# Kernel optimization log

Measured on AMD Instinct MI355X. Metric: run time of the kernel, lower is better.

## Reference

```python
import jax, jax.numpy as jnp
import numpy as np

B, LQ, LP, H = 16, 2048, 2048, 1024

def setup_inputs() -> dict:
    key = jax.random.key(0)
    kq, kp, kw = jax.random.split(key, 3)
    q = jax.random.normal(kq, (B, LQ, H), dtype=jnp.float32)
    p = jax.random.normal(kp, (B, LP, H), dtype=jnp.float32)
    W = jax.random.normal(kw, (H, H), dtype=jnp.float32) * (1.0 / np.sqrt(H))
    b = jnp.zeros((H,), dtype=jnp.float32)
    return {"q": q, "p": p, "W": W, "b": b}

def reference(q, p, W, b):
    # shared linear + ReLU projections (torch Linear: x @ W.T + b)
    q_lin = jax.nn.relu(jnp.einsum('bqh,oh->bqo', q, W) + b)  # [B,LQ,H]
    p_lin = jax.nn.relu(jnp.einsum('bph,oh->bpo', p, W) + b)  # [B,LP,H]
    # unscaled cross-attention scores: p_lin @ q_lin^T -> [B,LP,LQ]
    scores = jnp.einsum('bpd,bqd->bpq', p_lin, q_lin)
    att = jax.nn.softmax(scores, axis=2)
    # context-aware query: att @ q_lin -> [B,LP,H]
    return jnp.einsum('bpq,bqd->bpd', att, q_lin)
```

## Files before the change

### kernel.cpp

```cpp
#include <hip/hip_runtime.h>


#define LQN 2048
#define LPN 2048
#define HD  1024
#define NBATCH 16

typedef _Float16 half8 __attribute__((ext_vector_type(8)));
typedef _Float16 half4_t __attribute__((ext_vector_type(4)));
typedef float f32x4 __attribute__((ext_vector_type(4)));

#define GLP(src, dst) __builtin_amdgcn_global_load_lds(                          \
    (const __attribute__((address_space(1))) void*)(src),                        \
    (__attribute__((address_space(3))) void*)(dst), 16, 0, 0)

__global__ __launch_bounds__(256) void cvt_f32_f16(const float* __restrict__ in,
                                                   _Float16* __restrict__ out,
                                                   long n4) {
  long i0 = (long)blockIdx.x * blockDim.x + threadIdx.x;
  long stride = (long)gridDim.x * blockDim.x;
  for (long i = i0; i < n4; i += stride) {
    float4 v = ((const float4*)in)[i];
    half4_t h = {(_Float16)v.x, (_Float16)v.y, (_Float16)v.z, (_Float16)v.w};
    ((half4_t*)out)[i] = h;
  }
}

__global__ __launch_bounds__(256) void transpose_k(const _Float16* __restrict__ in,
                                                   _Float16* __restrict__ out) {
  __shared__ _Float16 t[64][72];
  const int bz = blockIdx.z;
  const int q0 = blockIdx.x * 64;
  const int d0 = blockIdx.y * 64;
  const int tt = threadIdx.x;
  const int ql = tt & 63, dg = tt >> 6;
  const _Float16* src = in + ((size_t)bz * LQN + q0 + ql) * HD + d0 + dg * 16;
  half8 v0 = *(const half8*)(src);
  half8 v1 = *(const half8*)(src + 8);
  int g0 = (dg * 2) ^ (ql & 7);
  int g1 = (dg * 2 + 1) ^ (ql & 7);
  *(half8*)&t[ql][g0 * 8] = v0;
  *(half8*)&t[ql][g1 * 8] = v1;
  __syncthreads();
  const int dl = tt & 63, qg = tt >> 6;
  half8 o0, o1;
#pragma unroll
  for (int j = 0; j < 8; ++j) {
    int qq = qg * 16 + j;
    o0[j] = t[qq][(((dl >> 3) ^ (qq & 7)) << 3) + (dl & 7)];
  }
#pragma unroll
  for (int j = 0; j < 8; ++j) {
    int qq = qg * 16 + 8 + j;
    o1[j] = t[qq][(((dl >> 3) ^ (qq & 7)) << 3) + (dl & 7)];
  }
  _Float16* dst = out + ((size_t)bz * HD + d0 + dl) * LQN + q0 + qg * 16;
  *(half8*)dst = o0;
  *(half8*)(dst + 8) = o1;
}


#define SYNC_PRE                                        \
  __builtin_amdgcn_s_barrier();                         \
  __builtin_amdgcn_s_setprio(1);

#define SYNC_POST                                       \
  __builtin_amdgcn_s_setprio(0);                        \
  __builtin_amdgcn_s_barrier();                         \
  __builtin_amdgcn_sched_barrier(0);

#define SYNC_POST_VM                                    \
  __builtin_amdgcn_s_setprio(0);                        \
  asm volatile("s_waitcnt vmcnt(4)" ::: "memory");      \
  __builtin_amdgcn_s_barrier();                         \
  __builtin_amdgcn_sched_barrier(0);

#define LOADA_TO(dst, qm, buf)                                                    \
  _Pragma("unroll")                                                               \
  for (int mi = 0; mi < 4; ++mi) {                                                \
    dst[mi][0] = *(const half8*)(smA + (buf)*32768 + a0 + ((qm)*4+mi)*4096);      \
    dst[mi][1] = *(const half8*)(smA + (buf)*32768 + a1 + ((qm)*4+mi)*4096);      \
  }

#define LOADB_TO(dst, qn, buf)                                                    \
  _Pragma("unroll")                                                               \
  for (int ni = 0; ni < 2; ++ni) {                                                \
    dst[ni][0] = *(const half8*)(smB + (buf)*32768 + b0 + ((qn)*2+ni)*8192);      \
    dst[ni][1] = *(const half8*)(smB + (buf)*32768 + b1 + ((qn)*2+ni)*8192);      \
  }

#define STAGEA(t, h, buf) do {                                                    \
  GLP(gA + (size_t)((h)*128)*lda + (size_t)(t)*64,                                \
      smW + (buf)*32768 + (h)*16384 + wid*1024);                                  \
  GLP(gA + (size_t)((h)*128+64)*lda + (size_t)(t)*64,                             \
      smW + (buf)*32768 + (h)*16384 + 8192 + wid*1024);                           \
} while (0)

#define STAGEB(t, h, buf) do {                                                    \
  GLP(gB + (size_t)((h)*128)*ldb + (size_t)(t)*64,                                \
      smW + 65536 + (buf)*32768 + (h)*16384 + wid*1024);                          \
  GLP(gB + (size_t)((h)*128+64)*ldb + (size_t)(t)*64,                             \
      smW + 65536 + (buf)*32768 + (h)*16384 + 8192 + wid*1024);                   \
} while (0)

#define DO_MFMA2(aset, bset, qm, qn)                                              \
  _Pragma("unroll")                                                               \
  for (int mi = 0; mi < 4; ++mi) {                                                \
    _Pragma("unroll")                                                             \
    for (int ni = 0; ni < 2; ++ni) {                                              \
      acc[(qm)*4+mi][(qn)*2+ni] = __builtin_amdgcn_mfma_f32_16x16x32_f16(         \
          aset[mi][0], bset[ni][0], acc[(qm)*4+mi][(qn)*2+ni], 0, 0, 0);          \
      acc[(qm)*4+mi][(qn)*2+ni] = __builtin_amdgcn_mfma_f32_16x16x32_f16(         \
          aset[mi][1], bset[ni][1], acc[(qm)*4+mi][(qn)*2+ni], 0, 0, 0);          \
    }                                                                             \
  }

template <int EPI>
__global__ __launch_bounds__(512, 2) void gemm8p(
    const _Float16* __restrict__ A, const _Float16* __restrict__ B,
    const float* __restrict__ bias, void* __restrict__ Cv,
    float2* __restrict__ side, int K, int lda, int ldb, int ldc,
    long sAz, long sBz, long sCz) {
  extern __shared__ __align__(16) char smem[];
  const char* smA = smem;
  const char* smB = smem + 65536;
  char* smW = smem;

  const int tid = threadIdx.x;
  const int lane = tid & 63, wid = tid >> 6;
  const int l16 = lane & 15, lhi = lane >> 4;
  const int wr = wid >> 2, wcn = wid & 3;

  const int nx = gridDim.x;
  const int d = blockIdx.y * nx + blockIdx.x;
  const int cpx = (nx * gridDim.y) >> 3;
  const int t_ = (d & 7) * cpx + (d >> 3);
  const int xsh = 31 - __builtin_clz(nx);
  const int bn0 = (t_ & (nx - 1)) << 8;
  const int bm0 = (t_ >> xsh) << 8;

  const int mask = (l16 & 7) << 4;
  const int a0 = (wr * 2048 + l16 * 128 + lhi * 16) ^ mask;
  const int a1 = a0 ^ 64;
  const int b0 = (wcn * 2048 + l16 * 128 + lhi * 16) ^ mask;
  const int b1 = b0 ^ 64;

  const int srow = tid >> 3;
  const int scol = (((tid & 7) ^ ((tid >> 3) & 7)) << 3);

  const _Float16* gA = A + (size_t)blockIdx.z * sAz + (size_t)(bm0 + srow) * lda + scol;
  const _Float16* gB = B + (size_t)blockIdx.z * sBz + (size_t)(bn0 + srow) * ldb + scol;

  const int NT = K >> 6, NI = K >> 7;

  f32x4 acc[8][4] = {};
  half8 aA[4][2], bs0[2][2], bs1[2][2];

  STAGEA(0, 0, 0); STAGEA(0, 1, 0); STAGEB(0, 0, 0); STAGEB(0, 1, 0);
  STAGEA(1, 0, 1); STAGEB(1, 0, 1);
  __builtin_amdgcn_sched_barrier(0);
  asm volatile("s_waitcnt vmcnt(4)" ::: "memory");
  __builtin_amdgcn_s_barrier();
  __builtin_amdgcn_sched_barrier(0);

  for (int i = 0; i < NI; ++i) {
    const int t1 = 2 * i + 1;
    int t2c = 2 * i + 2; if (t2c > NT - 1) t2c = NT - 1;
    int t3c = 2 * i + 3; if (t3c > NT - 1) t3c = NT - 1;
    STAGEA(t1, 1, 1); STAGEB(t1, 1, 1);
    LOADA_TO(aA, 0, 0) LOADB_TO(bs0, 0, 0) LOADB_TO(bs1, 1, 0)
    SYNC_PRE DO_MFMA2(aA, bs0, 0, 0) DO_MFMA2(aA, bs1, 0, 1) SYNC_POST
    STAGEA(t2c, 0, 0); STAGEB(t2c, 0, 0);
    LOADA_TO(aA, 1, 0)
    SYNC_PRE DO_MFMA2(aA, bs0, 1, 0) DO_MFMA2(aA, bs1, 1, 1) SYNC_POST_VM
    STAGEA(t2c, 1, 0); STAGEB(t2c, 1, 0);
    LOADA_TO(aA, 0, 1) LOADB_TO(bs0, 0, 1) LOADB_TO(bs1, 1, 1)
    SYNC_PRE DO_MFMA2(aA, bs0, 0, 0) DO_MFMA2(aA, bs1, 0, 1) SYNC_POST
    STAGEA(t3c, 0, 1); STAGEB(t3c, 0, 1);
    LOADA_TO(aA, 1, 1)
    SYNC_PRE DO_MFMA2(aA, bs0, 1, 0) DO_MFMA2(aA, bs1, 1, 1) SYNC_POST_VM
  }

  if constexpr (EPI == 0) {
    float* Cb = (float*)Cv + (size_t)blockIdx.z * sCz;
#pragma unroll
    for (int m = 0; m < 8; ++m) {
      int row0 = bm0 + m * 32 + wr * 16 + lhi * 4;
#pragma unroll
      for (int n = 0; n < 4; ++n) {
        int col = bn0 + n * 64 + wcn * 16 + l16;
#pragma unroll
        for (int v = 0; v < 4; ++v)
          Cb[(size_t)(row0 + v) * ldc + col] = acc[m][n][v];
      }
    }
  } else if constexpr (EPI == 1) {
    _Float16* Cb = (_Float16*)Cv;
#pragma unroll
    for (int n = 0; n < 4; ++n) {
      int col = bn0 + n * 64 + wcn * 16 + l16;
      float bv = bias[col];
#pragma unroll
      for (int m = 0; m < 8; ++m) {
        int row0 = bm0 + m * 32 + wr * 16 + lhi * 4;
        Cb[(size_t)(row0 + 0) * ldc + col] = (_Float16)fmaxf(acc[m][n][0] + bv, 0.f);
        Cb[(size_t)(row0 + 1) * ldc + col] = (_Float16)fmaxf(acc[m][n][1] + bv, 0.f);
        Cb[(size_t)(row0 + 2) * ldc + col] = (_Float16)fmaxf(acc[m][n][2] + bv, 0.f);
        Cb[(size_t)(row0 + 3) * ldc + col] = (_Float16)fmaxf(acc[m][n][3] + bv, 0.f);
      }
    }
  } else {
    float* redm = (float*)smW;
    float* reds = (float*)(smW + 4096);
    float tm[8][4];
#pragma unroll
    for (int m = 0; m < 8; ++m)
#pragma unroll
      for (int v = 0; v < 4; ++v)
        tm[m][v] = fmaxf(fmaxf(acc[m][0][v], acc[m][1][v]),
                         fmaxf(acc[m][2][v], acc[m][3][v]));
#pragma unroll
    for (int o = 1; o < 16; o <<= 1)
#pragma unroll
      for (int m = 0; m < 8; ++m)
#pragma unroll
        for (int v = 0; v < 4; ++v)
          tm[m][v] = fmaxf(tm[m][v], __shfl_xor(tm[m][v], o));
    __syncthreads();
    if (l16 == 0) {
#pragma unroll
      for (int m = 0; m < 8; ++m)
#pragma unroll
        for (int v = 0; v < 4; ++v)
          redm[(m * 32 + wr * 16 + lhi * 4 + v) * 4 + wcn] = tm[m][v];
    }
    __syncthreads();
    float rm[8][4], rs[8][4];
#pragma unroll
    for (int m = 0; m < 8; ++m)
#pragma unroll
      for (int v = 0; v < 4; ++v) {
        float4 q4 = ((const float4*)redm)[m * 32 + wr * 16 + lhi * 4 + v];
        rm[m][v] = fmaxf(fmaxf(q4.x, q4.y), fmaxf(q4.z, q4.w));
      }
#pragma unroll
    for (int m = 0; m < 8; ++m)
#pragma unroll
      for (int v = 0; v < 4; ++v) {
        float s = 0.f;
#pragma unroll
        for (int n = 0; n < 4; ++n) {
          float e = __expf(acc[m][n][v] - rm[m][v]);
          acc[m][n][v] = e;
          s += e;
        }
        tm[m][v] = s;
      }
#pragma unroll
    for (int o = 1; o < 16; o <<= 1)
#pragma unroll
      for (int m = 0; m < 8; ++m)
#pragma unroll
        for (int v = 0; v < 4; ++v)
          tm[m][v] += __shfl_xor(tm[m][v], o);
    __syncthreads();
    if (l16 == 0) {
#pragma unroll
      for (int m = 0; m < 8; ++m)
#pragma unroll
        for (int v = 0; v < 4; ++v)
          reds[(m * 32 + wr * 16 + lhi * 4 + v) * 4 + wcn] = tm[m][v];
    }
    __syncthreads();
#pragma unroll
    for (int m = 0; m < 8; ++m)
#pragma unroll
      for (int v = 0; v < 4; ++v) {
        float4 q4 = ((const float4*)reds)[m * 32 + wr * 16 + lhi * 4 + v];
        rs[m][v] = (q4.x + q4.y) + (q4.z + q4.w);
      }
    _Float16* Cb = (_Float16*)Cv + (size_t)blockIdx.z * sCz;
#pragma unroll
    for (int n = 0; n < 4; ++n) {
      int col = bn0 + n * 64 + wcn * 16 + l16;
#pragma unroll
      for (int m = 0; m < 8; ++m) {
        int row0 = bm0 + m * 32 + wr * 16 + lhi * 4;
        Cb[(size_t)(row0 + 0) * ldc + col] = (_Float16)acc[m][n][0];
        Cb[(size_t)(row0 + 1) * ldc + col] = (_Float16)acc[m][n][1];
        Cb[(size_t)(row0 + 2) * ldc + col] = (_Float16)acc[m][n][2];
        Cb[(size_t)(row0 + 3) * ldc + col] = (_Float16)acc[m][n][3];
      }
    }
    if (l16 == 0 && wcn == 0) {
      float2* sb = side + ((size_t)blockIdx.z * 2048 + bm0) * 8 + (bn0 >> 8);
#pragma unroll
      for (int m = 0; m < 8; ++m)
#pragma unroll
        for (int v = 0; v < 4; ++v) {
          int r = m * 32 + wr * 16 + lhi * 4 + v;
          sb[(size_t)r * 8] = make_float2(rm[m][v], rs[m][v]);
        }
    }
  }
}

__global__ __launch_bounds__(256) void renorm_k(_Float16* __restrict__ P,
                                                const float2* __restrict__ side) {
  const int row = blockIdx.x;
  const int bz = blockIdx.y;
  const float2* sd = side + ((size_t)bz * 2048 + row) * 8;
  float mt[8], st[8];
#pragma unroll
  for (int t = 0; t < 8; ++t) { float2 v = sd[t]; mt[t] = v.x; st[t] = v.y; }
  float m = mt[0];
#pragma unroll
  for (int t = 1; t < 8; ++t) m = fmaxf(m, mt[t]);
  float S = 0.f;
#pragma unroll
  for (int t = 0; t < 8; ++t) S += st[t] * __expf(mt[t] - m);
  const float inv = 1.f / S;
  const int tid = threadIdx.x;
  const float sc = __expf(mt[tid >> 5] - m) * inv;
  _Float16* p = P + (((size_t)bz * 2048 + row) * 2048) + tid * 8;
  half8 v = *(half8*)p;
#pragma unroll
  for (int j = 0; j < 8; ++j) v[j] = (_Float16)((float)v[j] * sc);
  *(half8*)p = v;
}

extern "C" void kernel_launch(void* const* d_in, const int* in_sizes, int n_in,
                              void* d_out, int out_size, void* d_ws, size_t ws_size,
                              hipStream_t stream) {
  const float* q = (const float*)d_in[0];
  const float* p = (const float*)d_in[1];
  const float* W = (const float*)d_in[2];
  const float* bias = (const float*)d_in[3];
  float* out = (float*)d_out;
  char* ws = (char*)d_ws;

  _Float16* qf    = (_Float16*)(ws);
  _Float16* pf    = (_Float16*)(ws + 67108864L);
  _Float16* qlin  = (_Float16*)(ws + 134217728L);
  _Float16* plin  = (_Float16*)(ws + 201326592L);
  _Float16* qlinT = (_Float16*)(ws + 268435456L);
  _Float16* Wf    = (_Float16*)(ws + 335544320L);
  _Float16* Pbuf  = (_Float16*)(ws);
  float2*   side  = (float2*)(ws + 67108864L);

  const long nQ = (long)NBATCH * LQN * HD;
  const size_t SH = 131072;

  cvt_f32_f16<<<2048, 256, 0, stream>>>(q, qf, nQ / 4);
  cvt_f32_f16<<<2048, 256, 0, stream>>>(p, pf, nQ / 4);
  cvt_f32_f16<<<64, 256, 0, stream>>>(W, Wf, (long)HD * HD / 4);

  gemm8p<1><<<dim3(HD / 256, 2 * NBATCH * LQN / 256, 1), 512, SH, stream>>>(
      qf, Wf, bias, qlin, (float2*)0, HD, HD, HD, HD, 0, 0, 0);

  transpose_k<<<dim3(LQN / 64, HD / 64, NBATCH), 256, 0, stream>>>(qlin, qlinT);

  for (int c = 0; c < 2; ++c) {
    int bz0 = c * 8;
    gemm8p<2><<<dim3(LQN / 256, LPN / 256, 8), 512, SH, stream>>>(
        plin + (size_t)bz0 * LPN * HD, qlin + (size_t)bz0 * LQN * HD,
        (const float*)0, Pbuf, side,
        HD, HD, HD, LQN,
        (long)LPN * HD, (long)LQN * HD, (long)LPN * LQN);
    renorm_k<<<dim3(LPN, 8), 256, 0, stream>>>(Pbuf, side);
    gemm8p<0><<<dim3(HD / 256, LPN / 256, 8), 512, SH, stream>>>(
        Pbuf, qlinT + (size_t)bz0 * HD * LQN,
        (const float*)0, out + (size_t)bz0 * LPN * HD, (float2*)0,
        LQN, LQN, LQN, HD,
        (long)LPN * LQN, (long)HD * LQN, (long)LPN * HD);
  }
}
```

Baseline: 593.1 us.

## Load GEMM B operand directly from global into registers, halve LDS

The GEMM mainloop no longer stages the B tile through shared memory. Each wave now loads its B fragments straight from global memory into registers, double-buffered across even and odd K tiles, while A is still staged with global_load_lds. Shared memory drops from 128KB to 64KB and the per-tile barrier pattern is simplified to one sync per tile. This trades LDS traffic and barriers for redundant global and L2 reads of B across waves that share columns, plus extra register pressure.

```diff
diff --git a/kernel.cpp b/kernel.cpp
--- a/kernel.cpp
+++ b/kernel.cpp
@@ -60,60 +60,45 @@
 }
 
 
-#define SYNC_PRE                                        \
-  __builtin_amdgcn_s_barrier();                         \
-  __builtin_amdgcn_s_setprio(1);
-
-#define SYNC_POST                                       \
-  __builtin_amdgcn_s_setprio(0);                        \
-  __builtin_amdgcn_s_barrier();                         \
-  __builtin_amdgcn_sched_barrier(0);
-
-#define SYNC_POST_VM                                    \
-  __builtin_amdgcn_s_setprio(0);                        \
-  asm volatile("s_waitcnt vmcnt(4)" ::: "memory");      \
-  __builtin_amdgcn_s_barrier();                         \
-  __builtin_amdgcn_sched_barrier(0);
-
-#define LOADA_TO(dst, qm, buf)                                                    \
+#define STAGEA_FULL(t, buf) do {                                                  \
+  GLP(gA + (size_t)(t)*64,                      smW + (buf)*32768 + wid*1024);    \
+  GLP(gA + (size_t)64*lda  + (size_t)(t)*64,    smW + (buf)*32768 +  8192 + wid*1024); \
+  GLP(gA + (size_t)128*lda + (size_t)(t)*64,    smW + (buf)*32768 + 16384 + wid*1024); \
+  GLP(gA + (size_t)192*lda + (size_t)(t)*64,    smW + (buf)*32768 + 24576 + wid*1024); \
+} while (0)
+
+#define LOADB_G(dst, t)                                                           \
+  _Pragma("unroll")                                                               \
+  for (int nb = 0; nb < 4; ++nb) {                                                \
+    dst[nb][0] = *(const half8*)(gBr + (size_t)(nb) * 64 * ldb + (size_t)(t)*64); \
+    dst[nb][1] = *(const half8*)(gBr + (size_t)(nb) * 64 * ldb + (size_t)(t)*64 + 32); \
+  }
+
+#define LOADA_H(qm, buf)                                                          \
   _Pragma("unroll")                                                               \
   for (int mi = 0; mi < 4; ++mi) {                                                \
-    dst[mi][0] = *(const half8*)(smA + (buf)*32768 + a0 + ((qm)*4+mi)*4096);      \
-    dst[mi][1] = *(const half8*)(smA + (buf)*32768 + a1 + ((qm)*4+mi)*4096);      \
-  }
-
-#define LOADB_TO(dst, qn, buf)                                                    \
-  _Pragma("unroll")                                                               \
-  for (int ni = 0; ni < 2; ++ni) {                                                \
-    dst[ni][0] = *(const half8*)(smB + (buf)*32768 + b0 + ((qn)*2+ni)*8192);      \
-    dst[ni][1] = *(const half8*)(smB + (buf)*32768 + b1 + ((qn)*2+ni)*8192);      \
-  }
-
-#define STAGEA(t, h, buf) do {                                                    \
-  GLP(gA + (size_t)((h)*128)*lda + (size_t)(t)*64,                                \
-      smW + (buf)*32768 + (h)*16384 + wid*1024);                                  \
-  GLP(gA + (size_t)((h)*128+64)*lda + (size_t)(t)*64,                             \
-      smW + (buf)*32768 + (h)*16384 + 8192 + wid*1024);                           \
-} while (0)
-
-#define STAGEB(t, h, buf) do {                                                    \
-  GLP(gB + (size_t)((h)*128)*ldb + (size_t)(t)*64,                                \
-      smW + 65536 + (buf)*32768 + (h)*16384 + wid*1024);                          \
-  GLP(gB + (size_t)((h)*128+64)*ldb + (size_t)(t)*64,                             \
-      smW + 65536 + (buf)*32768 + (h)*16384 + 8192 + wid*1024);                   \
-} while (0)
-
-#define DO_MFMA2(aset, bset, qm, qn)                                              \
+    aA[mi][0] = *(const half8*)(smA + (buf)*32768 + a0 + ((qm)*4+mi)*4096);       \
+    aA[mi][1] = *(const half8*)(smA + (buf)*32768 + a1 + ((qm)*4+mi)*4096);       \
+  }
+
+#define DO_HALF(qm, bs)                                                           \
   _Pragma("unroll")                                                               \
   for (int mi = 0; mi < 4; ++mi) {                                                \
     _Pragma("unroll")                                                             \
-    for (int ni = 0; ni < 2; ++ni) {                                              \
-      acc[(qm)*4+mi][(qn)*2+ni] = __builtin_amdgcn_mfma_f32_16x16x32_f16(         \
-          aset[mi][0], bset[ni][0], acc[(qm)*4+mi][(qn)*2+ni], 0, 0, 0);          \
-      acc[(qm)*4+mi][(qn)*2+ni] = __builtin_amdgcn_mfma_f32_16x16x32_f16(         \
-          aset[mi][1], bset[ni][1], acc[(qm)*4+mi][(qn)*2+ni], 0, 0, 0);          \
+    for (int nb = 0; nb < 4; ++nb) {                                              \
+      acc[(qm)*4+mi][nb] = __builtin_amdgcn_mfma_f32_16x16x32_f16(                \
+          aA[mi][0], bs[nb][0], acc[(qm)*4+mi][nb], 0, 0, 0);                     \
+      acc[(qm)*4+mi][nb] = __builtin_amdgcn_mfma_f32_16x16x32_f16(                \
+          aA[mi][1], bs[nb][1], acc[(qm)*4+mi][nb], 0, 0, 0);                     \
     }                                                                             \
   }
+
+#define TILE_SYNC                                       \
+  __builtin_amdgcn_s_setprio(0);                        \
+  __builtin_amdgcn_sched_barrier(0);                    \
+  asm volatile("s_waitcnt vmcnt(8)" ::: "memory");      \
+  __builtin_amdgcn_s_barrier();                         \
+  __builtin_amdgcn_sched_barrier(0);
 
 template <int EPI>
 __global__ __launch_bounds__(512, 2) void gemm8p(
@@ -123,7 +108,6 @@
     long sAz, long sBz, long sCz) {
   extern __shared__ __align__(16) char smem[];
   const char* smA = smem;
-  const char* smB = smem + 65536;
   char* smW = smem;
 
   const int tid = threadIdx.x;
@@ -142,44 +126,53 @@
   const int mask = (l16 & 7) << 4;
   const int a0 = (wr * 2048 + l16 * 128 + lhi * 16) ^ mask;
   const int a1 = a0 ^ 64;
-  const int b0 = (wcn * 2048 + l16 * 128 + lhi * 16) ^ mask;
-  const int b1 = b0 ^ 64;
 
   const int srow = tid >> 3;
   const int scol = (((tid & 7) ^ ((tid >> 3) & 7)) << 3);
 
   const _Float16* gA = A + (size_t)blockIdx.z * sAz + (size_t)(bm0 + srow) * lda + scol;
-  const _Float16* gB = B + (size_t)blockIdx.z * sBz + (size_t)(bn0 + srow) * ldb + scol;
+  const _Float16* gBr = B + (size_t)blockIdx.z * sBz +
+                        (size_t)(bn0 + wcn * 16 + l16) * ldb + lhi * 8;
 
   const int NT = K >> 6, NI = K >> 7;
 
   f32x4 acc[8][4] = {};
-  half8 aA[4][2], bs0[2][2], bs1[2][2];
-
-  STAGEA(0, 0, 0); STAGEA(0, 1, 0); STAGEB(0, 0, 0); STAGEB(0, 1, 0);
-  STAGEA(1, 0, 1); STAGEB(1, 0, 1);
-  __builtin_amdgcn_sched_barrier(0);
-  asm volatile("s_waitcnt vmcnt(4)" ::: "memory");
+  half8 aA[4][2], bsE[4][2], bsO[4][2];
+
+  STAGEA_FULL(0, 0);
+  __builtin_amdgcn_sched_barrier(0);
+  LOADB_G(bsE, 0)
+  __builtin_amdgcn_sched_barrier(0);
+  asm volatile("s_waitcnt vmcnt(8)" ::: "memory");
   __builtin_amdgcn_s_barrier();
   __builtin_amdgcn_sched_barrier(0);
 
   for (int i = 0; i < NI; ++i) {
-    const int t1 = 2 * i + 1;
-    int t2c = 2 * i + 2; if (t2c > NT - 1) t2c = NT - 1;
-    int t3c = 2 * i + 3; if (t3c > NT - 1) t3c = NT - 1;
-    STAGEA(t1, 1, 1); STAGEB(t1, 1, 1);
-    LOADA_TO(aA, 0, 0) LOADB_TO(bs0, 0, 0) LOADB_TO(bs1, 1, 0)
-    SYNC_PRE DO_MFMA2(aA, bs0, 0, 0) DO_MFMA2(aA, bs1, 0, 1) SYNC_POST
-    STAGEA(t2c, 0, 0); STAGEB(t2c, 0, 0);
-    LOADA_TO(aA, 1, 0)
-    SYNC_PRE DO_MFMA2(aA, bs0, 1, 0) DO_MFMA2(aA, bs1, 1, 1) SYNC_POST_VM
-    STAGEA(t2c, 1, 0); STAGEB(t2c, 1, 0);
-    LOADA_TO(aA, 0, 1) LOADB_TO(bs0, 0, 1) LOADB_TO(bs1, 1, 1)
-    SYNC_PRE DO_MFMA2(aA, bs0, 0, 0) DO_MFMA2(aA, bs1, 0, 1) SYNC_POST
-    STAGEA(t3c, 0, 1); STAGEB(t3c, 0, 1);
-    LOADA_TO(aA, 1, 1)
-    SYNC_PRE DO_MFMA2(aA, bs0, 1, 0) DO_MFMA2(aA, bs1, 1, 1) SYNC_POST_VM
-  }
+    const int tEn = 2 * i + 1;
+    int tOn = 2 * i + 2; if (tOn > NT - 1) tOn = NT - 1;
+    STAGEA_FULL(tEn, 1);
+    __builtin_amdgcn_sched_barrier(0);
+    LOADB_G(bsO, tEn)
+    LOADA_H(0, 0);
+    __builtin_amdgcn_s_setprio(1);
+    DO_HALF(0, bsE)
+    LOADA_H(1, 0);
+    DO_HALF(1, bsE)
+    TILE_SYNC
+    STAGEA_FULL(tOn, 0);
+    __builtin_amdgcn_sched_barrier(0);
+    LOADB_G(bsE, tOn)
+    LOADA_H(0, 1);
+    __builtin_amdgcn_s_setprio(1);
+    DO_HALF(0, bsO)
+    LOADA_H(1, 1);
+    DO_HALF(1, bsO)
+    TILE_SYNC
+  }
+
+  __builtin_amdgcn_sched_barrier(0);
+  asm volatile("s_waitcnt vmcnt(0)" ::: "memory");
+  __builtin_amdgcn_s_barrier();
 
   if constexpr (EPI == 0) {
     float* Cb = (float*)Cv + (size_t)blockIdx.z * sCz;
@@ -226,7 +219,6 @@
 #pragma unroll
         for (int v = 0; v < 4; ++v)
           tm[m][v] = fmaxf(tm[m][v], __shfl_xor(tm[m][v], o));
-    __syncthreads();
     if (l16 == 0) {
 #pragma unroll
       for (int m = 0; m < 8; ++m)
@@ -349,7 +341,7 @@
   float2*   side  = (float2*)(ws + 67108864L);
 
   const long nQ = (long)NBATCH * LQN * HD;
-  const size_t SH = 131072;
+  const size_t SH = 65536;
 
   cvt_f32_f16<<<2048, 256, 0, stream>>>(q, qf, nQ / 4);
   cvt_f32_f16<<<2048, 256, 0, stream>>>(p, pf, nQ / 4);
```

After: 804.5 us. 35.6% more time.
